# Performance work log

Hardware: AMD Instinct MI355X
Metric: run time of the kernel (lower is better)

## Reference

```python
import jax, jax.numpy as jnp
import numpy as np

N = 100000
E = 1600000
IN_DIM = 64
HID = 64


def _glorot(key, shape):
    fan_in, fan_out = shape[0], shape[1]
    lim = np.sqrt(6.0 / (fan_in + fan_out))
    return jax.random.uniform(key, shape, jnp.float32, -lim, lim)


def setup_inputs() -> dict:
    key = jax.random.key(0)
    ks = jax.random.split(key, 14)
    x = jax.random.normal(ks[0], (N, IN_DIM), jnp.float32)
    edge_index = jax.random.randint(ks[1], (2, E), 0, N, jnp.int64)
    dims = [(IN_DIM, HID), (HID, HID), (HID, HID), (HID, 1)]
    inp = {"x": x, "edge_index": edge_index}
    for i, (di, do) in enumerate(dims, start=1):
        inp[f"Wself{i}"] = _glorot(ks[2 + 3 * (i - 1)], (di, do))
        inp[f"Wneigh{i}"] = _glorot(ks[3 + 3 * (i - 1)], (di, do))
        inp[f"b{i}"] = jnp.zeros((do,), jnp.float32)
    return inp


def _gn_block(h, src, dst, deg_inv, Wself, Wneigh, b, act):
    # gather -> scatter-add -> mean -> dense transform (GraphConv-style)
    msg = h[src]                                           # [E, d]
    agg = jax.ops.segment_sum(msg, dst, num_segments=N)    # [N, d]
    agg = agg * deg_inv                                    # mean aggregation
    out = h @ Wself + agg @ Wneigh + b
    return act(out)


def reference(x, edge_index, Wself1, Wneigh1, b1, Wself2, Wneigh2, b2,
              Wself3, Wneigh3, b3, Wself4, Wneigh4, b4):
    src, dst = edge_index[0], edge_index[1]
    deg = jax.ops.segment_sum(jnp.ones((E,), x.dtype), dst, num_segments=N)
    deg_inv = (1.0 / jnp.maximum(deg, 1.0))[:, None]       # [N, 1]
    relu = jax.nn.relu
    h = _gn_block(x, src, dst, deg_inv, Wself1, Wneigh1, b1, relu)
    h = _gn_block(h, src, dst, deg_inv, Wself2, Wneigh2, b2, relu)
    h = _gn_block(h, src, dst, deg_inv, Wself3, Wneigh3, b3, relu)
    h = _gn_block(h, src, dst, deg_inv, Wself4, Wneigh4, b4, lambda z: z)
    return jax.nn.sigmoid(h)                               # [N, 1]
```

## Files before the change

kernel.cpp:

```cpp
#include <hip/hip_runtime.h>
#include <hip/hip_bf16.h>
#include <math.h>


using bfrag = __attribute__((ext_vector_type(8))) short;
using ffrag = __attribute__((ext_vector_type(4))) float;

#define BKT_SHIFT 9
#define BKT_NODES (1 << BKT_SHIFT)
#define AGG_STRIDE 72

__device__ __forceinline__ int load_idx32(const int* __restrict__ ei32, int is64,
                                          long long pos) {
    return is64 ? ei32[2 * pos] : ei32[pos];
}

__device__ __forceinline__ unsigned short f2b_rne(float f) {
    union { float f; unsigned u; } c;
    c.f = f;
    unsigned r = c.u + 0x7FFFu + ((c.u >> 16) & 1u);
    return (unsigned short)(r >> 16);
}

__device__ __forceinline__ float b2f(unsigned short u) {
    union { unsigned u; float f; } c;
    c.u = ((unsigned)u) << 16;
    return c.f;
}

__global__ void bprep_init_kernel(
    const float* __restrict__ Ws1, const float* __restrict__ Wn1,
    const float* __restrict__ Ws2, const float* __restrict__ Wn2,
    const float* __restrict__ Ws3, const float* __restrict__ Wn3,
    unsigned short* __restrict__ bthi, unsigned short* __restrict__ btlo,
    const int* __restrict__ ei, int* __restrict__ bktc, int* __restrict__ flag) {
    if (blockIdx.x == 0) {
        bktc[threadIdx.x] = 0;
        if (threadIdx.x == 0) {
            int allz = 1;
            for (int i = 0; i < 32; ++i)
                if (ei[2 * i + 1] != 0) allz = 0;
            *flag = allz;
        }
    }
    int i = blockIdx.x * 256 + threadIdx.x;
    if (i >= 3 * 8192) return;
    int layer = i >> 13;
    int j = i & 8191;
    int n = j >> 7, k = j & 127;
    const float* Ws = layer == 0 ? Ws1 : (layer == 1 ? Ws2 : Ws3);
    const float* Wn = layer == 0 ? Wn1 : (layer == 1 ? Wn2 : Wn3);
    float v = (k < 64) ? Ws[k * 64 + n] : Wn[(k - 64) * 64 + n];
    unsigned short hi = f2b_rne(v);
    bthi[i] = hi;
    btlo[i] = f2b_rne(v - b2f(hi));
}

__global__ void split_x_kernel(const float4* __restrict__ in, ushort4* __restrict__ hi,
                               int n4) {
    int i = blockIdx.x * blockDim.x + threadIdx.x;
    if (i >= n4) return;
    float4 v = in[i];
    ushort4 h;
    h.x = f2b_rne(v.x); h.y = f2b_rne(v.y); h.z = f2b_rne(v.z); h.w = f2b_rne(v.w);
    hi[i] = h;
}

__global__ __launch_bounds__(256) void binA_kernel(
    const int* __restrict__ ei32, const int* __restrict__ flagp,
    int* __restrict__ bktCnt, unsigned* __restrict__ bins, int E, int nbkt,
    int cap, int chunksz) {
    __shared__ int cnt[256];
    __shared__ int base[256];
    int is64 = *flagp;
    int elo = blockIdx.x * chunksz;
    int ehi = min(E, elo + chunksz);
    if (elo >= E) return;
    for (int i = threadIdx.x; i < nbkt; i += 256) cnt[i] = 0;
    __syncthreads();
    for (int e = elo + (int)threadIdx.x; e < ehi; e += 256) {
        int dst = load_idx32(ei32, is64, (long long)E + e);
        atomicAdd(&cnt[dst >> BKT_SHIFT], 1);
    }
    __syncthreads();
    for (int i = threadIdx.x; i < nbkt; i += 256) {
        base[i] = atomicAdd(&bktCnt[i], cnt[i]);
        cnt[i] = 0;
    }
    __syncthreads();
    for (int e = elo + (int)threadIdx.x; e < ehi; e += 256) {
        int dst = load_idx32(ei32, is64, (long long)E + e);
        int src = load_idx32(ei32, is64, e);
        int b = dst >> BKT_SHIFT;
        int r = atomicAdd(&cnt[b], 1);
        bins[(size_t)b * cap + base[b] + r] =
            ((unsigned)(dst & (BKT_NODES - 1)) << 23) | (unsigned)src;
    }
}

__global__ __launch_bounds__(256) void bucketCSR_kernel(
    const int* __restrict__ bktCnt, const unsigned* __restrict__ bins,
    int* __restrict__ off, int* __restrict__ offe, int* __restrict__ col,
    float* __restrict__ dinv, int N, int cap) {
    __shared__ int deg[BKT_NODES];
    __shared__ int loc[BKT_NODES];
    __shared__ int ssum[256];
    int b = blockIdx.x;
    int lo = b << BKT_SHIFT;
    int n = min(BKT_NODES, N - lo);
    for (int i = threadIdx.x; i < BKT_NODES; i += 256) deg[i] = 0;
    __syncthreads();
    int cnt = bktCnt[b];
    const unsigned* bb = bins + (size_t)b * cap;
    for (int i = threadIdx.x; i < cnt; i += 256)
        atomicAdd(&deg[bb[i] >> 23], 1);
    __syncthreads();
    int t = threadIdx.x;
    int d0 = deg[2 * t], d1 = deg[2 * t + 1];
    int s = d0 + d1;
    ssum[t] = s;
    __syncthreads();
    for (int o = 1; o < 256; o <<= 1) {
        int v = (t >= o) ? ssum[t - o] : 0;
        __syncthreads();
        ssum[t] += v;
        __syncthreads();
    }
    int excl = ssum[t] - s;
    loc[2 * t] = excl;
    loc[2 * t + 1] = excl + d0;
    __syncthreads();
    int base = b * cap;
    for (int i = threadIdx.x; i < n; i += 256) {
        int d = deg[i];
        off[lo + i] = base + loc[i];
        offe[lo + i] = base + loc[i] + d;
        dinv[lo + i] = 1.0f / fmaxf((float)d, 1.0f);
    }
    __syncthreads();
    for (int i = threadIdx.x; i < cnt; i += 256) {
        unsigned p = bb[i];
        int pos = atomicAdd(&loc[p >> 23], 1);
        col[base + pos] = (int)(p & 0x7FFFFFu);
    }
}

__device__ __forceinline__ void acc4(float4& a, ushort4 u) {
    a.x += b2f(u.x); a.y += b2f(u.y); a.z += b2f(u.z); a.w += b2f(u.w);
}

__device__ __forceinline__ void fma4(float4& a, float m, ushort4 u) {
    a.x = fmaf(m, b2f(u.x), a.x);
    a.y = fmaf(m, b2f(u.y), a.y);
    a.z = fmaf(m, b2f(u.z), a.z);
    a.w = fmaf(m, b2f(u.w), a.w);
}

__device__ __forceinline__ void gather_node_v3(
    const unsigned short* __restrict__ Hhi, const int* __restrict__ off,
    const int* __restrict__ offe, const int* __restrict__ col,
    const float* __restrict__ dinv, unsigned short* __restrict__ aggRow,
    int n, int N, int t16) {
    if (n >= N) {
        ushort4 z = make_ushort4(0, 0, 0, 0);
        *(ushort4*)&aggRow[t16 * 4] = z;
        return;
    }
    int e = off[n], end = offe[n];
    float4 a0 = make_float4(0.f, 0.f, 0.f, 0.f);
    float4 a1 = a0, a2 = a0, a3 = a0;
    const unsigned short* __restrict__ Hq = Hhi + t16 * 4;
    for (; e + 8 <= end; e += 8) {
        int s0 = col[e + 0], s1 = col[e + 1], s2 = col[e + 2], s3 = col[e + 3];
        int s4 = col[e + 4], s5 = col[e + 5], s6 = col[e + 6], s7 = col[e + 7];
        ushort4 u0 = *(const ushort4*)&Hq[(size_t)s0 * 64];
        ushort4 u1 = *(const ushort4*)&Hq[(size_t)s1 * 64];
        ushort4 u2 = *(const ushort4*)&Hq[(size_t)s2 * 64];
        ushort4 u3 = *(const ushort4*)&Hq[(size_t)s3 * 64];
        ushort4 u4 = *(const ushort4*)&Hq[(size_t)s4 * 64];
        ushort4 u5 = *(const ushort4*)&Hq[(size_t)s5 * 64];
        ushort4 u6 = *(const ushort4*)&Hq[(size_t)s6 * 64];
        ushort4 u7 = *(const ushort4*)&Hq[(size_t)s7 * 64];
        acc4(a0, u0); acc4(a1, u1); acc4(a2, u2); acc4(a3, u3);
        acc4(a0, u4); acc4(a1, u5); acc4(a2, u6); acc4(a3, u7);
    }
    int rem = end - e;
    if (rem > 0) {
        int last = end - 1;
#pragma unroll
        for (int j = 0; j < 7; ++j) {
            int idx = e + j;
            int cl = idx < last ? idx : last;
            int s = col[cl];
            ushort4 u = *(const ushort4*)&Hq[(size_t)s * 64];
            float m = (j < rem) ? 1.0f : 0.0f;
            if ((j & 3) == 0) fma4(a0, m, u);
            else if ((j & 3) == 1) fma4(a1, m, u);
            else if ((j & 3) == 2) fma4(a2, m, u);
            else fma4(a3, m, u);
        }
    }
    float4 acc;
    acc.x = (a0.x + a1.x) + (a2.x + a3.x);
    acc.y = (a0.y + a1.y) + (a2.y + a3.y);
    acc.z = (a0.z + a1.z) + (a2.z + a3.z);
    acc.w = (a0.w + a1.w) + (a2.w + a3.w);
    float di = dinv[n];
    ushort4 h;
    h.x = f2b_rne(acc.x * di);
    h.y = f2b_rne(acc.y * di);
    h.z = f2b_rne(acc.z * di);
    h.w = f2b_rne(acc.w * di);
    *(ushort4*)&aggRow[t16 * 4] = h;
}

__global__ __launch_bounds__(256) void layer_fused_kernel(
    const unsigned short* __restrict__ Hhi, const int* __restrict__ off,
    const int* __restrict__ offe, const int* __restrict__ col,
    const float* __restrict__ dinv,
    const unsigned short* __restrict__ Bthi, const unsigned short* __restrict__ Btlo,
    const float* __restrict__ b, unsigned short* __restrict__ Dhi, int N) {
    __shared__ unsigned short aggL[16 * AGG_STRIDE];
    int wave = threadIdx.x >> 6;
    int lane = threadIdx.x & 63;
    int g = lane >> 4;
    int t16 = lane & 15;
    int n0 = blockIdx.x * 16;
    int li = wave * 4 + g;
    gather_node_v3(Hhi, off, offe, col, dinv, aggL + li * AGG_STRIDE,
                   n0 + li, N, t16);
    __syncthreads();
    int m = t16, quad = g;
    int nr = n0 + m;
    if (nr > N - 1) nr = N - 1;
    const unsigned short* hrow = Hhi + (size_t)nr * 64 + quad * 8;
    bfrag ah[4];
    ah[0] = *(const bfrag*)(hrow);
    ah[1] = *(const bfrag*)(hrow + 32);
    ah[2] = *(const bfrag*)&aggL[m * AGG_STRIDE + quad * 8];
    ah[3] = *(const bfrag*)&aggL[m * AGG_STRIDE + 32 + quad * 8];
    int oc = wave * 16 + m;
    float bl = b[oc];
    ffrag acc = {bl, bl, bl, bl};
#pragma unroll
    for (int c = 0; c < 4; ++c) {
        bfrag bh = *(const bfrag*)(Bthi + (size_t)oc * 128 + c * 32 + quad * 8);
        bfrag bw = *(const bfrag*)(Btlo + (size_t)oc * 128 + c * 32 + quad * 8);
        acc = __builtin_amdgcn_mfma_f32_16x16x32_bf16(ah[c], bh, acc, 0, 0, 0);
        acc = __builtin_amdgcn_mfma_f32_16x16x32_bf16(ah[c], bw, acc, 0, 0, 0);
    }
#pragma unroll
    for (int r = 0; r < 4; ++r) {
        int node = n0 + quad * 4 + r;
        if (node < N)
            Dhi[(size_t)node * 64 + oc] = f2b_rne(fmaxf(acc[r], 0.f));
    }
}

__global__ __launch_bounds__(256) void layer_fused_last_kernel(
    const unsigned short* __restrict__ Hhi, const int* __restrict__ off,
    const int* __restrict__ offe, const int* __restrict__ col,
    const float* __restrict__ dinv,
    const unsigned short* __restrict__ Bthi, const unsigned short* __restrict__ Btlo,
    const float* __restrict__ b, const float* __restrict__ Ws4,
    const float* __restrict__ Wn4, float* __restrict__ sbuf,
    float* __restrict__ gbuf, int N) {
    __shared__ unsigned short aggL[16 * AGG_STRIDE];
    __shared__ float sPart[4][16];
    __shared__ float gPart[4][16];
    int wave = threadIdx.x >> 6;
    int lane = threadIdx.x & 63;
    int g = lane >> 4;
    int t16 = lane & 15;
    int n0 = blockIdx.x * 16;
    int li = wave * 4 + g;
    gather_node_v3(Hhi, off, offe, col, dinv, aggL + li * AGG_STRIDE,
                   n0 + li, N, t16);
    __syncthreads();
    int m = t16, quad = g;
    int nr = n0 + m;
    if (nr > N - 1) nr = N - 1;
    const unsigned short* hrow = Hhi + (size_t)nr * 64 + quad * 8;
    bfrag ah[4];
    ah[0] = *(const bfrag*)(hrow);
    ah[1] = *(const bfrag*)(hrow + 32);
    ah[2] = *(const bfrag*)&aggL[m * AGG_STRIDE + quad * 8];
    ah[3] = *(const bfrag*)&aggL[m * AGG_STRIDE + 32 + quad * 8];
    int oc = wave * 16 + m;
    float bl = b[oc];
    ffrag acc = {bl, bl, bl, bl};
#pragma unroll
    for (int c = 0; c < 4; ++c) {
        bfrag bh = *(const bfrag*)(Bthi + (size_t)oc * 128 + c * 32 + quad * 8);
        bfrag bw = *(const bfrag*)(Btlo + (size_t)oc * 128 + c * 32 + quad * 8);
        acc = __builtin_amdgcn_mfma_f32_16x16x32_bf16(ah[c], bh, acc, 0, 0, 0);
        acc = __builtin_amdgcn_mfma_f32_16x16x32_bf16(ah[c], bw, acc, 0, 0, 0);
    }
    float w4s = Ws4[oc], w4n = Wn4[oc];
#pragma unroll
    for (int r = 0; r < 4; ++r) {
        float v = fmaxf(acc[r], 0.f);
        float ps = v * w4s;
        float pg = v * w4n;
#pragma unroll
        for (int mask = 1; mask <= 8; mask <<= 1) {
            ps += __shfl_xor(ps, mask, 64);
            pg += __shfl_xor(pg, mask, 64);
        }
        if (m == 0) {
            sPart[wave][quad * 4 + r] = ps;
            gPart[wave][quad * 4 + r] = pg;
        }
    }
    __syncthreads();
    if (threadIdx.x < 16) {
        int node = n0 + threadIdx.x;
        if (node < N) {
            float s = sPart[0][threadIdx.x] + sPart[1][threadIdx.x] +
                      sPart[2][threadIdx.x] + sPart[3][threadIdx.x];
            float gg = gPart[0][threadIdx.x] + gPart[1][threadIdx.x] +
                       gPart[2][threadIdx.x] + gPart[3][threadIdx.x];
            sbuf[node] = s;
            gbuf[node] = gg;
        }
    }
}

__global__ void final_kernel(const float* __restrict__ s, const float* __restrict__ dinv,
                             const float* __restrict__ g, const int* __restrict__ off,
                             const int* __restrict__ offe, const int* __restrict__ col,
                             const float* __restrict__ b4, float* __restrict__ out, int N) {
    int n = blockIdx.x * blockDim.x + threadIdx.x;
    if (n >= N) return;
    float a = 0.f;
    int e = off[n], end = offe[n];
    for (; e < end; ++e) a += g[col[e]];
    float z = s[n] + dinv[n] * a + b4[0];
    out[n] = 1.0f / (1.0f + expf(-z));
}

static inline int cdiv(long long a, long long b) { return (int)((a + b - 1) / b); }

extern "C" void kernel_launch(void* const* d_in, const int* in_sizes, int n_in,
                              void* d_out, int out_size, void* d_ws, size_t ws_size,
                              hipStream_t stream) {
    const float* x   = (const float*)d_in[0];
    const int*   ei  = (const int*)d_in[1];
    const float* Ws1 = (const float*)d_in[2];
    const float* Wn1 = (const float*)d_in[3];
    const float* b1  = (const float*)d_in[4];
    const float* Ws2 = (const float*)d_in[5];
    const float* Wn2 = (const float*)d_in[6];
    const float* b2  = (const float*)d_in[7];
    const float* Ws3 = (const float*)d_in[8];
    const float* Wn3 = (const float*)d_in[9];
    const float* b3  = (const float*)d_in[10];
    const float* Ws4 = (const float*)d_in[11];
    const float* Wn4 = (const float*)d_in[12];
    const float* b4  = (const float*)d_in[13];
    float* out = (float*)d_out;

    const int N = in_sizes[0] / 64;
    const int E = in_sizes[1] / 2;

    const int nbkt = cdiv(N, BKT_NODES);
    const int cap  = E / nbkt + E / nbkt / 8 + 64;

    unsigned* bins = (unsigned*)d_ws;
    int* col = (int*)(bins + (size_t)nbkt * cap);
    unsigned short* HhiA = (unsigned short*)(col + (size_t)nbkt * cap);
    unsigned short* HhiB = HhiA + (size_t)N * 64;
    unsigned short* Bth  = HhiB + (size_t)N * 64;
    unsigned short* Btl  = Bth + 3 * 8192;
    float* dinv = (float*)(Btl + 3 * 8192);
    float* sbuf = dinv + N;
    float* gbuf = sbuf + N;
    int*   off  = (int*)(gbuf + N);
    int*   offe = off + N;
    int*   bktc = offe + N;
    int*   flag = bktc + 256;

    const int BT = 256;
    const int gridN  = cdiv(N, BT);
    const int gridL  = cdiv(N, 16);
    const int binBlocks = 512;
    const int chunksz = cdiv(E, binBlocks);

    bprep_init_kernel<<<96, BT, 0, stream>>>(Ws1, Wn1, Ws2, Wn2, Ws3, Wn3,
                                             Bth, Btl, ei, bktc, flag);
    split_x_kernel<<<cdiv((long long)N * 16, BT), BT, 0, stream>>>(
        (const float4*)x, (ushort4*)HhiA, N * 16);

    binA_kernel<<<binBlocks, BT, 0, stream>>>(ei, flag, bktc, bins, E, nbkt, cap, chunksz);
    bucketCSR_kernel<<<nbkt, BT, 0, stream>>>(bktc, bins, off, offe, col, dinv, N, cap);

    layer_fused_kernel<<<gridL, BT, 0, stream>>>(HhiA, off, offe, col, dinv,
                                                 Bth, Btl, b1, HhiB, N);
    layer_fused_kernel<<<gridL, BT, 0, stream>>>(HhiB, off, offe, col, dinv,
                                                 Bth + 8192, Btl + 8192, b2, HhiA, N);
    layer_fused_last_kernel<<<gridL, BT, 0, stream>>>(HhiA, off, offe, col, dinv,
                                                      Bth + 16384, Btl + 16384, b3,
                                                      Ws4, Wn4, sbuf, gbuf, N);

    final_kernel<<<gridN, BT, 0, stream>>>(sbuf, dinv, gbuf, off, offe, col, b4, out, N);
}
```

Measured before the change: 361.3 us.

## Stage binned edges in LDS for coalesced writes, deepen gather unroll, set occupancy

The binning kernel now processes fixed 2000-edge chunks and sorts each chunk's packed edges by bucket in shared memory, using a block prefix scan over bucket counts, before writing each bucket's run contiguously to global memory. This replaces scattered per-edge global stores with coalesced per-bucket copies, at the cost of extra syncs and a serial log-step scan. The neighbour gather loop is unrolled to 16 outstanding loads to raise memory-level parallelism. The layer kernels gain a min-blocks launch bound of 5, which may limit registers.

```diff
diff --git a/kernel.cpp b/kernel.cpp
--- a/kernel.cpp
+++ b/kernel.cpp
@@ -9,6 +9,8 @@
 #define BKT_SHIFT 9
 #define BKT_NODES (1 << BKT_SHIFT)
 #define AGG_STRIDE 72
+#define BIN_CHUNK 2000
+#define STAGE_CAP 2048
 
 __device__ __forceinline__ int load_idx32(const int* __restrict__ ei32, int is64,
                                           long long pos) {
@@ -69,32 +71,51 @@
 __global__ __launch_bounds__(256) void binA_kernel(
     const int* __restrict__ ei32, const int* __restrict__ flagp,
     int* __restrict__ bktCnt, unsigned* __restrict__ bins, int E, int nbkt,
-    int cap, int chunksz) {
+    int cap) {
     __shared__ int cnt[256];
+    __shared__ int cnt2[256];
     __shared__ int base[256];
+    __shared__ int lofs[256];
+    __shared__ unsigned stage[STAGE_CAP];
     int is64 = *flagp;
-    int elo = blockIdx.x * chunksz;
-    int ehi = min(E, elo + chunksz);
+    int elo = blockIdx.x * BIN_CHUNK;
     if (elo >= E) return;
-    for (int i = threadIdx.x; i < nbkt; i += 256) cnt[i] = 0;
-    __syncthreads();
-    for (int e = elo + (int)threadIdx.x; e < ehi; e += 256) {
+    int ehi = min(E, elo + BIN_CHUNK);
+    int t = threadIdx.x;
+    cnt[t] = 0;
+    __syncthreads();
+    for (int e = elo + t; e < ehi; e += 256) {
         int dst = load_idx32(ei32, is64, (long long)E + e);
         atomicAdd(&cnt[dst >> BKT_SHIFT], 1);
     }
     __syncthreads();
-    for (int i = threadIdx.x; i < nbkt; i += 256) {
-        base[i] = atomicAdd(&bktCnt[i], cnt[i]);
-        cnt[i] = 0;
-    }
-    __syncthreads();
-    for (int e = elo + (int)threadIdx.x; e < ehi; e += 256) {
+    int c = cnt[t];
+    cnt2[t] = c;
+    base[t] = atomicAdd(&bktCnt[t], c);
+    lofs[t] = c;
+    __syncthreads();
+    for (int o = 1; o < 256; o <<= 1) {
+        int v = (t >= o) ? lofs[t - o] : 0;
+        __syncthreads();
+        lofs[t] += v;
+        __syncthreads();
+    }
+    cnt[t] = lofs[t] - c;
+    __syncthreads();
+    for (int e = elo + t; e < ehi; e += 256) {
         int dst = load_idx32(ei32, is64, (long long)E + e);
         int src = load_idx32(ei32, is64, e);
         int b = dst >> BKT_SHIFT;
-        int r = atomicAdd(&cnt[b], 1);
-        bins[(size_t)b * cap + base[b] + r] =
-            ((unsigned)(dst & (BKT_NODES - 1)) << 23) | (unsigned)src;
+        int p = atomicAdd(&cnt[b], 1);
+        stage[p] = ((unsigned)(dst & (BKT_NODES - 1)) << 23) | (unsigned)src;
+    }
+    __syncthreads();
+    int wave = t >> 6, lane = t & 63;
+    for (int i = wave; i < nbkt; i += 4) {
+        int s = lofs[i] - cnt2[i];
+        int cc = cnt2[i];
+        unsigned* __restrict__ dstp = bins + (size_t)i * cap + base[i];
+        for (int j = lane; j < cc; j += 64) dstp[j] = stage[s + j];
     }
 }
 
@@ -156,7 +177,7 @@
     a.w = fmaf(m, b2f(u.w), a.w);
 }
 
-__device__ __forceinline__ void gather_node_v3(
+__device__ __forceinline__ void gather_node(
     const unsigned short* __restrict__ Hhi, const int* __restrict__ off,
     const int* __restrict__ offe, const int* __restrict__ col,
     const float* __restrict__ dinv, unsigned short* __restrict__ aggRow,
@@ -170,7 +191,33 @@
     float4 a0 = make_float4(0.f, 0.f, 0.f, 0.f);
     float4 a1 = a0, a2 = a0, a3 = a0;
     const unsigned short* __restrict__ Hq = Hhi + t16 * 4;
-    for (; e + 8 <= end; e += 8) {
+    for (; e + 16 <= end; e += 16) {
+        int s0 = col[e + 0],  s1 = col[e + 1],  s2 = col[e + 2],  s3 = col[e + 3];
+        int s4 = col[e + 4],  s5 = col[e + 5],  s6 = col[e + 6],  s7 = col[e + 7];
+        int s8 = col[e + 8],  s9 = col[e + 9],  s10 = col[e + 10], s11 = col[e + 11];
+        int s12 = col[e + 12], s13 = col[e + 13], s14 = col[e + 14], s15 = col[e + 15];
+        ushort4 u0 = *(const ushort4*)&Hq[(size_t)s0 * 64];
+        ushort4 u1 = *(const ushort4*)&Hq[(size_t)s1 * 64];
+        ushort4 u2 = *(const ushort4*)&Hq[(size_t)s2 * 64];
+        ushort4 u3 = *(const ushort4*)&Hq[(size_t)s3 * 64];
+        ushort4 u4 = *(const ushort4*)&Hq[(size_t)s4 * 64];
+        ushort4 u5 = *(const ushort4*)&Hq[(size_t)s5 * 64];
+        ushort4 u6 = *(const ushort4*)&Hq[(size_t)s6 * 64];
+        ushort4 u7 = *(const ushort4*)&Hq[(size_t)s7 * 64];
+        ushort4 u8 = *(const ushort4*)&Hq[(size_t)s8 * 64];
+        ushort4 u9 = *(const ushort4*)&Hq[(size_t)s9 * 64];
+        ushort4 u10 = *(const ushort4*)&Hq[(size_t)s10 * 64];
+        ushort4 u11 = *(const ushort4*)&Hq[(size_t)s11 * 64];
+        ushort4 u12 = *(const ushort4*)&Hq[(size_t)s12 * 64];
+        ushort4 u13 = *(const ushort4*)&Hq[(size_t)s13 * 64];
+        ushort4 u14 = *(const ushort4*)&Hq[(size_t)s14 * 64];
+        ushort4 u15 = *(const ushort4*)&Hq[(size_t)s15 * 64];
+        acc4(a0, u0);  acc4(a1, u1);  acc4(a2, u2);  acc4(a3, u3);
+        acc4(a0, u4);  acc4(a1, u5);  acc4(a2, u6);  acc4(a3, u7);
+        acc4(a0, u8);  acc4(a1, u9);  acc4(a2, u10); acc4(a3, u11);
+        acc4(a0, u12); acc4(a1, u13); acc4(a2, u14); acc4(a3, u15);
+    }
+    if (e + 8 <= end) {
         int s0 = col[e + 0], s1 = col[e + 1], s2 = col[e + 2], s3 = col[e + 3];
         int s4 = col[e + 4], s5 = col[e + 5], s6 = col[e + 6], s7 = col[e + 7];
         ushort4 u0 = *(const ushort4*)&Hq[(size_t)s0 * 64];
@@ -183,6 +230,7 @@
         ushort4 u7 = *(const ushort4*)&Hq[(size_t)s7 * 64];
         acc4(a0, u0); acc4(a1, u1); acc4(a2, u2); acc4(a3, u3);
         acc4(a0, u4); acc4(a1, u5); acc4(a2, u6); acc4(a3, u7);
+        e += 8;
     }
     int rem = end - e;
     if (rem > 0) {
@@ -214,7 +262,7 @@
     *(ushort4*)&aggRow[t16 * 4] = h;
 }
 
-__global__ __launch_bounds__(256) void layer_fused_kernel(
+__global__ __launch_bounds__(256, 5) void layer_fused_kernel(
     const unsigned short* __restrict__ Hhi, const int* __restrict__ off,
     const int* __restrict__ offe, const int* __restrict__ col,
     const float* __restrict__ dinv,
@@ -227,8 +275,8 @@
     int t16 = lane & 15;
     int n0 = blockIdx.x * 16;
     int li = wave * 4 + g;
-    gather_node_v3(Hhi, off, offe, col, dinv, aggL + li * AGG_STRIDE,
-                   n0 + li, N, t16);
+    gather_node(Hhi, off, offe, col, dinv, aggL + li * AGG_STRIDE,
+                n0 + li, N, t16);
     __syncthreads();
     int m = t16, quad = g;
     int nr = n0 + m;
@@ -257,7 +305,7 @@
     }
 }
 
-__global__ __launch_bounds__(256) void layer_fused_last_kernel(
+__global__ __launch_bounds__(256, 5) void layer_fused_last_kernel(
     const unsigned short* __restrict__ Hhi, const int* __restrict__ off,
     const int* __restrict__ offe, const int* __restrict__ col,
     const float* __restrict__ dinv,
@@ -274,8 +322,8 @@
     int t16 = lane & 15;
     int n0 = blockIdx.x * 16;
     int li = wave * 4 + g;
-    gather_node_v3(Hhi, off, offe, col, dinv, aggL + li * AGG_STRIDE,
-                   n0 + li, N, t16);
+    gather_node(Hhi, off, offe, col, dinv, aggL + li * AGG_STRIDE,
+                n0 + li, N, t16);
     __syncthreads();
     int m = t16, quad = g;
     int nr = n0 + m;
@@ -383,15 +431,14 @@
     const int BT = 256;
     const int gridN  = cdiv(N, BT);
     const int gridL  = cdiv(N, 16);
-    const int binBlocks = 512;
-    const int chunksz = cdiv(E, binBlocks);
+    const int binBlocks = cdiv(E, BIN_CHUNK);
 
     bprep_init_kernel<<<96, BT, 0, stream>>>(Ws1, Wn1, Ws2, Wn2, Ws3, Wn3,
                                              Bth, Btl, ei, bktc, flag);
     split_x_kernel<<<cdiv((long long)N * 16, BT), BT, 0, stream>>>(
         (const float4*)x, (ushort4*)HhiA, N * 16);
 
-    binA_kernel<<<binBlocks, BT, 0, stream>>>(ei, flag, bktc, bins, E, nbkt, cap, chunksz);
+    binA_kernel<<<binBlocks, BT, 0, stream>>>(ei, flag, bktc, bins, E, nbkt, cap);
     bucketCSR_kernel<<<nbkt, BT, 0, stream>>>(bktc, bins, off, offe, col, dinv, N, cap);
 
     layer_fused_kernel<<<gridL, BT, 0, stream>>>(HhiA, off, offe, col, dinv,
```

Result: slower. 383.5 us (+6.2%).

## Split each node's neighbor gather across two 16-lane groups with 512-thread blocks

Applied to the files above, without the earlier changes.

The fused layer kernels now use 512-thread blocks. Each node's edge range is split in half across two 16-lane groups, which write fp32 partial sums to shared memory. The first four waves then combine the halves, apply the degree inverse, round to bf16 and run the MFMA transform. CSR offsets are also packed into a single int2 array, so one load replaces two. The aim is more memory-level parallelism in the latency-bound gather, at the cost of extra shared memory, waves that sit idle during the MFMA phase, and larger blocks.

```diff
diff --git a/kernel.cpp b/kernel.cpp
--- a/kernel.cpp
+++ b/kernel.cpp
@@ -8,7 +8,7 @@
 
 #define BKT_SHIFT 9
 #define BKT_NODES (1 << BKT_SHIFT)
-#define AGG_STRIDE 72
+#define AGG_F_STRIDE 65
 
 __device__ __forceinline__ int load_idx32(const int* __restrict__ ei32, int is64,
                                           long long pos) {
@@ -100,7 +100,7 @@
 
 __global__ __launch_bounds__(256) void bucketCSR_kernel(
     const int* __restrict__ bktCnt, const unsigned* __restrict__ bins,
-    int* __restrict__ off, int* __restrict__ offe, int* __restrict__ col,
+    int2* __restrict__ offp, int* __restrict__ col,
     float* __restrict__ dinv, int N, int cap) {
     __shared__ int deg[BKT_NODES];
     __shared__ int loc[BKT_NODES];
@@ -133,8 +133,7 @@
     int base = b * cap;
     for (int i = threadIdx.x; i < n; i += 256) {
         int d = deg[i];
-        off[lo + i] = base + loc[i];
-        offe[lo + i] = base + loc[i] + d;
+        offp[lo + i] = make_int2(base + loc[i], base + loc[i] + d);
         dinv[lo + i] = 1.0f / fmaxf((float)d, 1.0f);
     }
     __syncthreads();
@@ -156,17 +155,9 @@
     a.w = fmaf(m, b2f(u.w), a.w);
 }
 
-__device__ __forceinline__ void gather_node_v3(
-    const unsigned short* __restrict__ Hhi, const int* __restrict__ off,
-    const int* __restrict__ offe, const int* __restrict__ col,
-    const float* __restrict__ dinv, unsigned short* __restrict__ aggRow,
-    int n, int N, int t16) {
-    if (n >= N) {
-        ushort4 z = make_ushort4(0, 0, 0, 0);
-        *(ushort4*)&aggRow[t16 * 4] = z;
-        return;
-    }
-    int e = off[n], end = offe[n];
+__device__ __forceinline__ void gather_half(
+    const unsigned short* __restrict__ Hhi, const int* __restrict__ col,
+    float* __restrict__ dstF, int e, int end, int t16) {
     float4 a0 = make_float4(0.f, 0.f, 0.f, 0.f);
     float4 a1 = a0, a2 = a0, a3 = a0;
     const unsigned short* __restrict__ Hq = Hhi + t16 * 4;
@@ -200,72 +191,87 @@
             else fma4(a3, m, u);
         }
     }
-    float4 acc;
-    acc.x = (a0.x + a1.x) + (a2.x + a3.x);
-    acc.y = (a0.y + a1.y) + (a2.y + a3.y);
-    acc.z = (a0.z + a1.z) + (a2.z + a3.z);
-    acc.w = (a0.w + a1.w) + (a2.w + a3.w);
-    float di = dinv[n];
-    ushort4 h;
-    h.x = f2b_rne(acc.x * di);
-    h.y = f2b_rne(acc.y * di);
-    h.z = f2b_rne(acc.z * di);
-    h.w = f2b_rne(acc.w * di);
-    *(ushort4*)&aggRow[t16 * 4] = h;
-}
-
-__global__ __launch_bounds__(256) void layer_fused_kernel(
-    const unsigned short* __restrict__ Hhi, const int* __restrict__ off,
-    const int* __restrict__ offe, const int* __restrict__ col,
-    const float* __restrict__ dinv,
+    float4 s;
+    s.x = (a0.x + a1.x) + (a2.x + a3.x);
+    s.y = (a0.y + a1.y) + (a2.y + a3.y);
+    s.z = (a0.z + a1.z) + (a2.z + a3.z);
+    s.w = (a0.w + a1.w) + (a2.w + a3.w);
+    *(float4*)&dstF[t16 * 4] = s;
+}
+
+__device__ __forceinline__ bfrag cvt8(const float* __restrict__ p0,
+                                      const float* __restrict__ p1, float di) {
+    bfrag r;
+#pragma unroll
+    for (int i = 0; i < 8; ++i)
+        r[i] = (short)f2b_rne((p0[i] + p1[i]) * di);
+    return r;
+}
+
+__global__ __launch_bounds__(512, 8) void layer_fused_kernel(
+    const unsigned short* __restrict__ Hhi, const int2* __restrict__ offp,
+    const int* __restrict__ col, const float* __restrict__ dinv,
     const unsigned short* __restrict__ Bthi, const unsigned short* __restrict__ Btlo,
     const float* __restrict__ b, unsigned short* __restrict__ Dhi, int N) {
-    __shared__ unsigned short aggL[16 * AGG_STRIDE];
+    __shared__ float aggF[32 * AGG_F_STRIDE];
     int wave = threadIdx.x >> 6;
     int lane = threadIdx.x & 63;
     int g = lane >> 4;
     int t16 = lane & 15;
     int n0 = blockIdx.x * 16;
-    int li = wave * 4 + g;
-    gather_node_v3(Hhi, off, offe, col, dinv, aggL + li * AGG_STRIDE,
-                   n0 + li, N, t16);
-    __syncthreads();
-    int m = t16, quad = g;
-    int nr = n0 + m;
-    if (nr > N - 1) nr = N - 1;
-    const unsigned short* hrow = Hhi + (size_t)nr * 64 + quad * 8;
-    bfrag ah[4];
-    ah[0] = *(const bfrag*)(hrow);
-    ah[1] = *(const bfrag*)(hrow + 32);
-    ah[2] = *(const bfrag*)&aggL[m * AGG_STRIDE + quad * 8];
-    ah[3] = *(const bfrag*)&aggL[m * AGG_STRIDE + 32 + quad * 8];
-    int oc = wave * 16 + m;
-    float bl = b[oc];
-    ffrag acc = {bl, bl, bl, bl};
-#pragma unroll
-    for (int c = 0; c < 4; ++c) {
-        bfrag bh = *(const bfrag*)(Bthi + (size_t)oc * 128 + c * 32 + quad * 8);
-        bfrag bw = *(const bfrag*)(Btlo + (size_t)oc * 128 + c * 32 + quad * 8);
-        acc = __builtin_amdgcn_mfma_f32_16x16x32_bf16(ah[c], bh, acc, 0, 0, 0);
-        acc = __builtin_amdgcn_mfma_f32_16x16x32_bf16(ah[c], bw, acc, 0, 0, 0);
-    }
-#pragma unroll
-    for (int r = 0; r < 4; ++r) {
-        int node = n0 + quad * 4 + r;
-        if (node < N)
-            Dhi[(size_t)node * 64 + oc] = f2b_rne(fmaxf(acc[r], 0.f));
-    }
-}
-
-__global__ __launch_bounds__(256) void layer_fused_last_kernel(
-    const unsigned short* __restrict__ Hhi, const int* __restrict__ off,
-    const int* __restrict__ offe, const int* __restrict__ col,
-    const float* __restrict__ dinv,
+    int grp = wave * 4 + g;
+    int li = grp >> 1, half = grp & 1;
+    int n = n0 + li;
+    int e0 = 0, e1 = 0;
+    if (n < N) {
+        int2 oo = offp[n];
+        int d = oo.y - oo.x;
+        int c0 = (d + 1) >> 1;
+        e0 = half ? oo.x + c0 : oo.x;
+        e1 = half ? oo.y : oo.x + c0;
+    }
+    gather_half(Hhi, col, &aggF[grp * AGG_F_STRIDE], e0, e1, t16);
+    __syncthreads();
+    if (wave < 4) {
+        int m = t16, quad = g;
+        int nr = n0 + m;
+        if (nr > N - 1) nr = N - 1;
+        float di = dinv[nr];
+        const float* r0 = &aggF[(m * 2 + 0) * AGG_F_STRIDE];
+        const float* r1 = &aggF[(m * 2 + 1) * AGG_F_STRIDE];
+        const unsigned short* hrow = Hhi + (size_t)nr * 64 + quad * 8;
+        bfrag ah[4];
+        ah[0] = *(const bfrag*)(hrow);
+        ah[1] = *(const bfrag*)(hrow + 32);
+        ah[2] = cvt8(r0 + quad * 8, r1 + quad * 8, di);
+        ah[3] = cvt8(r0 + 32 + quad * 8, r1 + 32 + quad * 8, di);
+        int oc = wave * 16 + m;
+        float bl = b[oc];
+        ffrag acc = {bl, bl, bl, bl};
+#pragma unroll
+        for (int c = 0; c < 4; ++c) {
+            bfrag bh = *(const bfrag*)(Bthi + (size_t)oc * 128 + c * 32 + quad * 8);
+            bfrag bw = *(const bfrag*)(Btlo + (size_t)oc * 128 + c * 32 + quad * 8);
+            acc = __builtin_amdgcn_mfma_f32_16x16x32_bf16(ah[c], bh, acc, 0, 0, 0);
+            acc = __builtin_amdgcn_mfma_f32_16x16x32_bf16(ah[c], bw, acc, 0, 0, 0);
+        }
+#pragma unroll
+        for (int r = 0; r < 4; ++r) {
+            int node = n0 + quad * 4 + r;
+            if (node < N)
+                Dhi[(size_t)node * 64 + oc] = f2b_rne(fmaxf(acc[r], 0.f));
+        }
+    }
+}
+
+__global__ __launch_bounds__(512, 8) void layer_fused_last_kernel(
+    const unsigned short* __restrict__ Hhi, const int2* __restrict__ offp,
+    const int* __restrict__ col, const float* __restrict__ dinv,
     const unsigned short* __restrict__ Bthi, const unsigned short* __restrict__ Btlo,
     const float* __restrict__ b, const float* __restrict__ Ws4,
     const float* __restrict__ Wn4, float* __restrict__ sbuf,
     float* __restrict__ gbuf, int N) {
-    __shared__ unsigned short aggL[16 * AGG_STRIDE];
+    __shared__ float aggF[32 * AGG_F_STRIDE];
     __shared__ float sPart[4][16];
     __shared__ float gPart[4][16];
     int wave = threadIdx.x >> 6;
@@ -273,43 +279,57 @@
     int g = lane >> 4;
     int t16 = lane & 15;
     int n0 = blockIdx.x * 16;
-    int li = wave * 4 + g;
-    gather_node_v3(Hhi, off, offe, col, dinv, aggL + li * AGG_STRIDE,
-                   n0 + li, N, t16);
-    __syncthreads();
-    int m = t16, quad = g;
-    int nr = n0 + m;
-    if (nr > N - 1) nr = N - 1;
-    const unsigned short* hrow = Hhi + (size_t)nr * 64 + quad * 8;
-    bfrag ah[4];
-    ah[0] = *(const bfrag*)(hrow);
-    ah[1] = *(const bfrag*)(hrow + 32);
-    ah[2] = *(const bfrag*)&aggL[m * AGG_STRIDE + quad * 8];
-    ah[3] = *(const bfrag*)&aggL[m * AGG_STRIDE + 32 + quad * 8];
-    int oc = wave * 16 + m;
-    float bl = b[oc];
-    ffrag acc = {bl, bl, bl, bl};
-#pragma unroll
-    for (int c = 0; c < 4; ++c) {
-        bfrag bh = *(const bfrag*)(Bthi + (size_t)oc * 128 + c * 32 + quad * 8);
-        bfrag bw = *(const bfrag*)(Btlo + (size_t)oc * 128 + c * 32 + quad * 8);
-        acc = __builtin_amdgcn_mfma_f32_16x16x32_bf16(ah[c], bh, acc, 0, 0, 0);
-        acc = __builtin_amdgcn_mfma_f32_16x16x32_bf16(ah[c], bw, acc, 0, 0, 0);
-    }
-    float w4s = Ws4[oc], w4n = Wn4[oc];
-#pragma unroll
-    for (int r = 0; r < 4; ++r) {
-        float v = fmaxf(acc[r], 0.f);
-        float ps = v * w4s;
-        float pg = v * w4n;
-#pragma unroll
-        for (int mask = 1; mask <= 8; mask <<= 1) {
-            ps += __shfl_xor(ps, mask, 64);
-            pg += __shfl_xor(pg, mask, 64);
-        }
-        if (m == 0) {
-            sPart[wave][quad * 4 + r] = ps;
-            gPart[wave][quad * 4 + r] = pg;
+    int grp = wave * 4 + g;
+    int li = grp >> 1, half = grp & 1;
+    int n = n0 + li;
+    int e0 = 0, e1 = 0;
+    if (n < N) {
+        int2 oo = offp[n];
+        int d = oo.y - oo.x;
+        int c0 = (d + 1) >> 1;
+        e0 = half ? oo.x + c0 : oo.x;
+        e1 = half ? oo.y : oo.x + c0;
+    }
+    gather_half(Hhi, col, &aggF[grp * AGG_F_STRIDE], e0, e1, t16);
+    __syncthreads();
+    if (wave < 4) {
+        int m = t16, quad = g;
+        int nr = n0 + m;
+        if (nr > N - 1) nr = N - 1;
+        float di = dinv[nr];
+        const float* r0 = &aggF[(m * 2 + 0) * AGG_F_STRIDE];
+        const float* r1 = &aggF[(m * 2 + 1) * AGG_F_STRIDE];
+        const unsigned short* hrow = Hhi + (size_t)nr * 64 + quad * 8;
+        bfrag ah[4];
+        ah[0] = *(const bfrag*)(hrow);
+        ah[1] = *(const bfrag*)(hrow + 32);
+        ah[2] = cvt8(r0 + quad * 8, r1 + quad * 8, di);
+        ah[3] = cvt8(r0 + 32 + quad * 8, r1 + 32 + quad * 8, di);
+        int oc = wave * 16 + m;
+        float bl = b[oc];
+        ffrag acc = {bl, bl, bl, bl};
+#pragma unroll
+        for (int c = 0; c < 4; ++c) {
+            bfrag bh = *(const bfrag*)(Bthi + (size_t)oc * 128 + c * 32 + quad * 8);
+            bfrag bw = *(const bfrag*)(Btlo + (size_t)oc * 128 + c * 32 + quad * 8);
+            acc = __builtin_amdgcn_mfma_f32_16x16x32_bf16(ah[c], bh, acc, 0, 0, 0);
+            acc = __builtin_amdgcn_mfma_f32_16x16x32_bf16(ah[c], bw, acc, 0, 0, 0);
+        }
+        float w4s = Ws4[oc], w4n = Wn4[oc];
+#pragma unroll
+        for (int r = 0; r < 4; ++r) {
+            float v = fmaxf(acc[r], 0.f);
+            float ps = v * w4s;
+            float pg = v * w4n;
+#pragma unroll
+            for (int mask = 1; mask <= 8; mask <<= 1) {
+                ps += __shfl_xor(ps, mask, 64);
+                pg += __shfl_xor(pg, mask, 64);
+            }
+            if (m == 0) {
+                sPart[wave][quad * 4 + r] = ps;
+                gPart[wave][quad * 4 + r] = pg;
+            }
         }
     }
     __syncthreads();
@@ -327,14 +347,14 @@
 }
 
 __global__ void final_kernel(const float* __restrict__ s, const float* __restrict__ dinv,
-                             const float* __restrict__ g, const int* __restrict__ off,
-                             const int* __restrict__ offe, const int* __restrict__ col,
+                             const float* __restrict__ g, const int2* __restrict__ offp,
+                             const int* __restrict__ col,
                              const float* __restrict__ b4, float* __restrict__ out, int N) {
     int n = blockIdx.x * blockDim.x + threadIdx.x;
     if (n >= N) return;
     float a = 0.f;
-    int e = off[n], end = offe[n];
-    for (; e < end; ++e) a += g[col[e]];
+    int2 oo = offp[n];
+    for (int e = oo.x; e < oo.y; ++e) a += g[col[e]];
     float z = s[n] + dinv[n] * a + b4[0];
     out[n] = 1.0f / (1.0f + expf(-z));
 }
@@ -364,20 +384,20 @@
     const int E = in_sizes[1] / 2;
 
     const int nbkt = cdiv(N, BKT_NODES);
-    const int cap  = E / nbkt + E / nbkt / 8 + 64;
+    int cap = E / nbkt + E / nbkt / 8 + 64;
+    cap = (cap + 1) & ~1;
 
     unsigned* bins = (unsigned*)d_ws;
     int* col = (int*)(bins + (size_t)nbkt * cap);
-    unsigned short* HhiA = (unsigned short*)(col + (size_t)nbkt * cap);
+    int2* offp = (int2*)(col + (size_t)nbkt * cap);
+    unsigned short* HhiA = (unsigned short*)(offp + N);
     unsigned short* HhiB = HhiA + (size_t)N * 64;
     unsigned short* Bth  = HhiB + (size_t)N * 64;
     unsigned short* Btl  = Bth + 3 * 8192;
     float* dinv = (float*)(Btl + 3 * 8192);
     float* sbuf = dinv + N;
     float* gbuf = sbuf + N;
-    int*   off  = (int*)(gbuf + N);
-    int*   offe = off + N;
-    int*   bktc = offe + N;
+    int*   bktc = (int*)(gbuf + N);
     int*   flag = bktc + 256;
 
     const int BT = 256;
@@ -392,15 +412,15 @@
         (const float4*)x, (ushort4*)HhiA, N * 16);
 
     binA_kernel<<<binBlocks, BT, 0, stream>>>(ei, flag, bktc, bins, E, nbkt, cap, chunksz);
-    bucketCSR_kernel<<<nbkt, BT, 0, stream>>>(bktc, bins, off, offe, col, dinv, N, cap);
-
-    layer_fused_kernel<<<gridL, BT, 0, stream>>>(HhiA, off, offe, col, dinv,
-                                                 Bth, Btl, b1, HhiB, N);
-    layer_fused_kernel<<<gridL, BT, 0, stream>>>(HhiB, off, offe, col, dinv,
-                                                 Bth + 8192, Btl + 8192, b2, HhiA, N);
-    layer_fused_last_kernel<<<gridL, BT, 0, stream>>>(HhiA, off, offe, col, dinv,
-                                                      Bth + 16384, Btl + 16384, b3,
-                                                      Ws4, Wn4, sbuf, gbuf, N);
-
-    final_kernel<<<gridN, BT, 0, stream>>>(sbuf, dinv, gbuf, off, offe, col, b4, out, N);
-}
+    bucketCSR_kernel<<<nbkt, BT, 0, stream>>>(bktc, bins, offp, col, dinv, N, cap);
+
+    layer_fused_kernel<<<gridL, 512, 0, stream>>>(HhiA, offp, col, dinv,
+                                                  Bth, Btl, b1, HhiB, N);
+    layer_fused_kernel<<<gridL, 512, 0, stream>>>(HhiB, offp, col, dinv,
+                                                  Bth + 8192, Btl + 8192, b2, HhiA, N);
+    layer_fused_last_kernel<<<gridL, 512, 0, stream>>>(HhiA, offp, col, dinv,
+                                                       Bth + 16384, Btl + 16384, b3,
+                                                       Ws4, Wn4, sbuf, gbuf, N);
+
+    final_kernel<<<gridN, BT, 0, stream>>>(sbuf, dinv, gbuf, offp, col, b4, out, N);
+}
```

After: 343.2 us. 1.05x faster.
